# Kernel tuning notes

Hardware: AMD Instinct MI355X
Metric: run time of the kernel (lower is better)

## Reference

```python
import jax, jax.numpy as jnp
import numpy as np

GRID = (15, 15)
HW = GRID[0] * GRID[1]
IMAGE_SIZE = 240
TEMP = 0.07
EPS = 1e-12


def make_masks(h, w, k):
    grid = np.arange(h * w).reshape(h, w)
    # matches torch unfold: kernel offsets row-major, spatial positions row-major
    idx = np.stack([grid[i:i + h - k + 1, j:j + w - k + 1] for i in range(k) for j in range(k)])
    return jnp.asarray(idx.reshape(k * k, -1), dtype=jnp.int32)  # [k*k, n_masks]


def _l2n(x):
    return x / jnp.maximum(jnp.linalg.norm(x, axis=-1, keepdims=True), EPS)


def cosine_sim(a, b):
    # a: [..., N, D], b: [M, D] -> [..., N, M]
    return jnp.einsum('...nd,md->...nm', _l2n(a), _l2n(b))


def harmonic_aggregation(window_scores, masks):
    # window_scores: [B, n_masks]; masks: [k2, n_masks] flat patch indices
    n_masks = masks.shape[1]
    # membership matrix M[p, w] = 1 if patch p is covered by window w
    M = jnp.zeros((HW, n_masks), dtype=window_scores.dtype)
    M = M.at[masks, jnp.arange(n_masks)[None, :]].set(1.0)
    counts = M.sum(axis=1)                                  # [HW]
    sums = (1.0 / window_scores) @ M.T                      # [B, HW]
    scores = counts[None, :] / sums
    scores = jnp.nan_to_num(scores, nan=0.0, posinf=0.0)
    return scores.reshape(-1, GRID[0], GRID[1])


def visual_association_score(embeds, ref_embeds):
    # embeds: [B, N, D]; ref_embeds: [K, N, D]
    flat = ref_embeds.reshape(-1, embeds.shape[-1])          # [K*N, D]
    scores = cosine_sim(embeds, flat)                        # [B, N, K*N]
    return (1.0 - scores).min(axis=-1) / 2.0                 # [B, N]


def setup_inputs() -> dict:
    key = jax.random.key(0)
    ks = jax.random.split(key, 8)
    B, D, K = 256, 640, 4
    return {
        'image_embeds': jax.random.normal(ks[0], (B, D), jnp.float32),
        'window_embeds_s2': jax.random.normal(ks[1], (B, 196, D), jnp.float32),
        'window_embeds_s3': jax.random.normal(ks[2], (B, 169, D), jnp.float32),
        'patch_embeds': jax.random.normal(ks[3], (B, 225, D), jnp.float32),
        'text_embeds': jax.random.normal(ks[4], (2, D), jnp.float32),
        'ref_patch_embeds': jax.random.normal(ks[5], (K, 225, D), jnp.float32),
        'ref_window_s2': jax.random.normal(ks[6], (K, 196, D), jnp.float32),
        'ref_window_s3': jax.random.normal(ks[7], (K, 169, D), jnp.float32),
        'masks_s2': make_masks(GRID[0], GRID[1], 2),
        'masks_s3': make_masks(GRID[0], GRID[1], 3),
    }


def reference(image_embeds, window_embeds_s2, window_embeds_s3, patch_embeds,
              text_embeds, ref_patch_embeds, ref_window_s2, ref_window_s3,
              masks_s2, masks_s3):
    B = image_embeds.shape[0]
    # image-level zero-shot anomaly score
    img_probs = jax.nn.softmax(cosine_sim(image_embeds, text_embeds) / TEMP, axis=-1)
    image_scores = img_probs[..., 1]                         # [B]

    # zero-shot multi-scale (harmonic mean of image score + window scores)
    zs = [jnp.broadcast_to(image_scores[:, None, None], (B, GRID[0], GRID[1]))]
    for we, m in ((window_embeds_s2, masks_s2), (window_embeds_s3, masks_s3)):
        s = jax.nn.softmax(cosine_sim(we, text_embeds) / TEMP, axis=-1)[..., 1]  # [B, n_masks]
        zs.append(harmonic_aggregation(s, m))
    zero_shot = len(zs) / (1.0 / jnp.stack(zs)).sum(axis=0)   # [B, H, W]

    # few-shot scores
    fs = [visual_association_score(patch_embeds, ref_patch_embeds).reshape(B, GRID[0], GRID[1])]
    for we, re, m in ((window_embeds_s2, ref_window_s2, masks_s2),
                      (window_embeds_s3, ref_window_s3, masks_s3)):
        fs.append(harmonic_aggregation(visual_association_score(we, re), m))
    few_shot = jnp.stack(fs).mean(axis=0)                     # [B, H, W]

    multi_scale = (zero_shot + few_shot) / 2.0
    image_scores = (image_scores + few_shot.max(axis=(-2, -1))) / 2.0
    pixel_scores = jax.image.resize(multi_scale, (B, IMAGE_SIZE, IMAGE_SIZE), method='bilinear')
    return image_scores, pixel_scores
```

## Files before the change

### kernel.cpp

```cpp
#include <hip/hip_runtime.h>
#include <cmath>

#define D 640
#define TEMP_INV (1.0f / 0.07f)

typedef __attribute__((ext_vector_type(8))) short bf16x8;
typedef __attribute__((ext_vector_type(4))) float f32x4;

__device__ __forceinline__ short f2bf(float f) {
    unsigned int u = __float_as_uint(f);
    unsigned int r = (u + 0x7fffu + ((u >> 16) & 1u)) >> 16;
    return (short)r;
}

__device__ __forceinline__ void gload_lds16(const void* g, void* l) {
    __builtin_amdgcn_global_load_lds(
        (const __attribute__((address_space(1))) unsigned int*)g,
        (__attribute__((address_space(3))) unsigned int*)l, 16, 0, 0);
}

__global__ void textnorm_k(const float* __restrict__ T, float* __restrict__ tn) {
    int w = threadIdx.x >> 6, lane = threadIdx.x & 63;
    const float* row = T + w * D;
    float v[10]; float ss = 0.f;
#pragma unroll
    for (int i = 0; i < 10; i++) { v[i] = row[lane + 64 * i]; ss += v[i] * v[i]; }
#pragma unroll
    for (int m = 1; m < 64; m <<= 1) ss += __shfl_xor(ss, m, 64);
    float rn = 1.f / fmaxf(sqrtf(ss), 1e-12f);
#pragma unroll
    for (int i = 0; i < 10; i++) tn[w * D + lane + 64 * i] = v[i] * rn;
}

__global__ __launch_bounds__(256) void normstore_k(
    const float* __restrict__ X, int nsrc, int npad, const float* __restrict__ tn,
    float* __restrict__ score_out, short* __restrict__ bf16_out) {
    int wid = blockIdx.x * 4 + (threadIdx.x >> 6);
    int lane = threadIdx.x & 63;
    if (wid >= npad) return;
    const float2* row = (const float2*)(X + (size_t)(wid < nsrc ? wid : 0) * D);
    const float2* t0 = (const float2*)tn;
    const float2* t1 = (const float2*)(tn + D);
    float2 v[5]; float ss = 0.f, d0 = 0.f, d1 = 0.f;
#pragma unroll
    for (int i = 0; i < 5; i++) {
        float2 a = row[lane + 64 * i];
        v[i] = a;
        ss += a.x * a.x + a.y * a.y;
        if (tn) {
            float2 b0 = t0[lane + 64 * i], b1 = t1[lane + 64 * i];
            d0 += a.x * b0.x + a.y * b0.y;
            d1 += a.x * b1.x + a.y * b1.y;
        }
    }
#pragma unroll
    for (int m = 1; m < 64; m <<= 1) {
        ss += __shfl_xor(ss, m, 64);
        if (tn) { d0 += __shfl_xor(d0, m, 64); d1 += __shfl_xor(d1, m, 64); }
    }
    float rn = 1.f / fmaxf(sqrtf(ss), 1e-12f);
    if (score_out && lane == 0)
        score_out[wid] = 1.f / (1.f + expf(-((d1 - d0) * rn) * TEMP_INV));
    if (bf16_out) {
        ushort2* o = (ushort2*)bf16_out;
#pragma unroll
        for (int i = 0; i < 5; i++) {
            ushort2 p;
            p.x = (unsigned short)f2bf(v[i].x * rn);
            p.y = (unsigned short)f2bf(v[i].y * rn);
            o[(size_t)wid * 320 + lane + 64 * i] = p;
        }
    }
}

__global__ __launch_bounds__(512, 4) void gemm_max_k(
    const short* __restrict__ A, const short* __restrict__ B,
    int nch, int U, float* __restrict__ partial) {
    __shared__ short Al[128 * 64];
    __shared__ short Bl[256 * 64];
    const int t = threadIdx.x;
    const int g = blockIdx.x & 7, ii = blockIdx.x >> 3;
    const int ulo = (int)(((long long)g * U) >> 3);
    const int uhi = (int)(((long long)(g + 1) * U) >> 3);
    const int S = uhi - ulo;
    if (ii >= S) return;
    const int cnt = (S - ii + 63) >> 6;
    const int nchq = nch * 4;

    const int srow = t >> 3;
    const int scol = (t & 7) * 16;
    const int gsw = (scol ^ ((srow & 7) << 4)) >> 1;

    const int lane = t & 63, wave = t >> 6;
    const int l15 = lane & 15, lhi = lane >> 4;
    const int wr = wave >> 2, wc = wave & 3;
    const int xk = (l15 & 7) << 4;

    char* Ab = (char*)Al;
    char* Bb = (char*)Bl;
    char* Ad = Ab + srow * 128 + scol;
    char* Bd = Bb + srow * 128 + scol;

    for (int j = 0; j < cnt; j++) {
        const int u = ulo + ii + (j << 6);
        const int rc = u / nch, nc = u - rc * nch;
        const short* Ag = A + ((size_t)rc * 128 + srow) * D + gsw;
        const short* Bg = B + ((size_t)nc * 256 + srow) * D + gsw;

        f32x4 acc[4][4];
#pragma unroll
        for (int m = 0; m < 4; m++)
#pragma unroll
            for (int n = 0; n < 4; n++) acc[m][n] = (f32x4){0.f, 0.f, 0.f, 0.f};

        for (int ks = 0; ks < 10; ks++) {
            const int k0 = ks * 64;
            __syncthreads();
#pragma unroll
            for (int i = 0; i < 2; i++)
                gload_lds16(Ag + k0 + (size_t)(i * 64) * D, Ad + i * 8192);
#pragma unroll
            for (int i = 0; i < 4; i++)
                gload_lds16(Bg + k0 + (size_t)(i * 64) * D, Bd + i * 8192);
            __syncthreads();
#pragma unroll
            for (int sub = 0; sub < 2; sub++) {
                const int kbs = (sub * 64 + lhi * 16) ^ xk;
                bf16x8 a[4], b[4];
#pragma unroll
                for (int m = 0; m < 4; m++)
                    a[m] = *(const bf16x8*)(Ab + (wr * 64 + m * 16 + l15) * 128 + kbs);
#pragma unroll
                for (int n = 0; n < 4; n++)
                    b[n] = *(const bf16x8*)(Bb + (wc * 64 + n * 16 + l15) * 128 + kbs);
#pragma unroll
                for (int m = 0; m < 4; m++)
#pragma unroll
                    for (int n = 0; n < 4; n++)
                        acc[m][n] = __builtin_amdgcn_mfma_f32_16x16x32_bf16(a[m], b[n], acc[m][n], 0, 0, 0);
            }
        }

#pragma unroll
        for (int m = 0; m < 4; m++)
#pragma unroll
            for (int r = 0; r < 4; r++) {
                float v = fmaxf(fmaxf(acc[m][0][r], acc[m][1][r]),
                                fmaxf(acc[m][2][r], acc[m][3][r]));
#pragma unroll
                for (int msk = 1; msk < 16; msk <<= 1)
                    v = fmaxf(v, __shfl_xor(v, msk, 64));
                if (l15 == 0) {
                    int row = rc * 128 + wr * 64 + m * 16 + lhi * 4 + r;
                    partial[(size_t)row * nchq + nc * 4 + wc] = v;
                }
            }
    }
}

__global__ __launch_bounds__(256) void reducemax_k(
    const float* __restrict__ partial, int nchq, int nrows, float* __restrict__ vas) {
    int r = blockIdx.x * 256 + threadIdx.x;
    if (r >= nrows) return;
    float m = -1e30f;
    for (int i = 0; i < nchq; i++) m = fmaxf(m, partial[(size_t)r * nchq + i]);
    vas[r] = (1.0f - m) * 0.5f;
}

__global__ __launch_bounds__(256) void rowstats_k(
    const float* __restrict__ X, int nrows, const float* __restrict__ tn,
    float* __restrict__ rnorm_out, float* __restrict__ score_out) {
    int wid = blockIdx.x * 4 + (threadIdx.x >> 6);
    int lane = threadIdx.x & 63;
    if (wid >= nrows) return;
    const float* row = X + (size_t)wid * D;
    float ss = 0.f, d0 = 0.f, d1 = 0.f;
#pragma unroll
    for (int i = 0; i < 10; i++) {
        float v = row[lane + 64 * i];
        ss += v * v;
        if (tn) { d0 += v * tn[lane + 64 * i]; d1 += v * tn[D + lane + 64 * i]; }
    }
#pragma unroll
    for (int m = 1; m < 64; m <<= 1) {
        ss += __shfl_xor(ss, m, 64);
        if (tn) { d0 += __shfl_xor(d0, m, 64); d1 += __shfl_xor(d1, m, 64); }
    }
    if (lane == 0) {
        float rn = 1.f / fmaxf(sqrtf(ss), 1e-12f);
        if (rnorm_out) rnorm_out[wid] = rn;
        if (score_out) score_out[wid] = 1.f / (1.f + expf(-((d1 - d0) * rn) * TEMP_INV));
    }
}

__global__ __launch_bounds__(256) void refnorm_k(
    const float* __restrict__ R, int M, int Mp, short* __restrict__ out) {
    int wid = blockIdx.x * 4 + (threadIdx.x >> 6);
    int lane = threadIdx.x & 63;
    if (wid >= Mp) return;
    const float* row = R + (size_t)(wid < M ? wid : 0) * D;
    float v[10]; float ss = 0.f;
#pragma unroll
    for (int i = 0; i < 10; i++) { v[i] = row[lane + 64 * i]; ss += v[i] * v[i]; }
#pragma unroll
    for (int m = 1; m < 64; m <<= 1) ss += __shfl_xor(ss, m, 64);
    float rn = 1.f / fmaxf(sqrtf(ss), 1e-12f);
#pragma unroll
    for (int i = 0; i < 10; i++) out[(size_t)wid * D + lane + 64 * i] = f2bf(v[i] * rn);
}

#define SA 648
#define SB 72
__global__ __launch_bounds__(256) void maxcos_k(
    const float* __restrict__ X, const float* __restrict__ rnorm,
    const short* __restrict__ refs, int Mp, float* __restrict__ vas_out) {
    __shared__ short Alds[64 * SA];
    __shared__ short Blds[64 * SB];
    const int t = threadIdx.x;
    const size_t rowBase = (size_t)blockIdx.x * 64;
#pragma unroll
    for (int i = 0; i < 20; i++) {
        int c = i * 256 + t;
        int row = c / 80, col = (c % 80) * 8;
        const float* p = X + (rowBase + row) * D + col;
        float rn = rnorm[rowBase + row];
        float4 v0 = *(const float4*)p;
        float4 v1 = *(const float4*)(p + 4);
        bf16x8 s;
        s[0] = f2bf(v0.x * rn); s[1] = f2bf(v0.y * rn);
        s[2] = f2bf(v0.z * rn); s[3] = f2bf(v0.w * rn);
        s[4] = f2bf(v1.x * rn); s[5] = f2bf(v1.y * rn);
        s[6] = f2bf(v1.z * rn); s[7] = f2bf(v1.w * rn);
        *(bf16x8*)&Alds[row * SA + col] = s;
    }
    __syncthreads();
    const int lane = t & 63, wave = t >> 6;
    const int l15 = lane & 15, lhi = lane >> 4;
    const int wr0 = wave * 16;
    float rowmax[4] = {-1e30f, -1e30f, -1e30f, -1e30f};
    for (int m0 = 0; m0 < Mp; m0 += 64) {
        f32x4 zero = {0.f, 0.f, 0.f, 0.f};
        f32x4 acc[4] = {zero, zero, zero, zero};
        for (int ks = 0; ks < 10; ks++) {
            __syncthreads();
#pragma unroll
            for (int c2 = 0; c2 < 2; c2++) {
                int c = c2 * 256 + t;
                int n = c >> 3, kk = (c & 7) * 8;
                const short* g = refs + (size_t)(m0 + n) * D + ks * 64 + kk;
                *(bf16x8*)&Blds[n * SB + kk] = *(const bf16x8*)g;
            }
            __syncthreads();
#pragma unroll
            for (int sub = 0; sub < 2; sub++) {
                bf16x8 a = *(const bf16x8*)&Alds[(wr0 + l15) * SA + ks * 64 + sub * 32 + lhi * 8];
#pragma unroll
                for (int s = 0; s < 4; s++) {
                    bf16x8 b = *(const bf16x8*)&Blds[(s * 16 + l15) * SB + sub * 32 + lhi * 8];
                    acc[s] = __builtin_amdgcn_mfma_f32_16x16x32_bf16(a, b, acc[s], 0, 0, 0);
                }
            }
        }
#pragma unroll
        for (int r = 0; r < 4; r++) {
            float mv = fmaxf(fmaxf(acc[0][r], acc[1][r]), fmaxf(acc[2][r], acc[3][r]));
#pragma unroll
            for (int msk = 1; msk < 16; msk <<= 1) mv = fmaxf(mv, __shfl_xor(mv, msk, 64));
            rowmax[r] = fmaxf(rowmax[r], mv);
        }
    }
    if (l15 == 0) {
#pragma unroll
        for (int r = 0; r < 4; r++) {
            size_t row = rowBase + wr0 + lhi * 4 + r;
            vas_out[row] = (1.0f - rowmax[r]) * 0.5f;
        }
    }
}

__global__ __launch_bounds__(256) void fuse_k(
    const float* __restrict__ imgsc, const float* __restrict__ zs2,
    const float* __restrict__ zs3, const float* __restrict__ vasP,
    const float* __restrict__ vas2, const float* __restrict__ vas3,
    float* __restrict__ multi, float* __restrict__ img_out) {
    int b = blockIdx.x, t = threadIdx.x;
    __shared__ float red[256];
    float few = -1e30f;
    if (t < 225) {
        int i = t / 15, j = t % 15;
        float invz2 = 0.f, invf2 = 0.f; int c2 = 0;
        int ilo = max(0, i - 1), ihi = min(i, 13), jlo = max(0, j - 1), jhi = min(j, 13);
        for (int i0 = ilo; i0 <= ihi; i0++)
            for (int j0 = jlo; j0 <= jhi; j0++) {
                int w = b * 196 + i0 * 14 + j0;
                invz2 += 1.f / zs2[w]; invf2 += 1.f / vas2[w]; c2++;
            }
        float zh2 = (float)c2 / invz2, fh2 = (float)c2 / invf2;
        float invz3 = 0.f, invf3 = 0.f; int c3 = 0;
        ilo = max(0, i - 2); ihi = min(i, 12); jlo = max(0, j - 2); jhi = min(j, 12);
        for (int i0 = ilo; i0 <= ihi; i0++)
            for (int j0 = jlo; j0 <= jhi; j0++) {
                int w = b * 169 + i0 * 13 + j0;
                invz3 += 1.f / zs3[w]; invf3 += 1.f / vas3[w]; c3++;
            }
        float zh3 = (float)c3 / invz3, fh3 = (float)c3 / invf3;
        float is = imgsc[b];
        float zero_shot = 3.f / (1.f / is + 1.f / zh2 + 1.f / zh3);
        float fs0 = vasP[b * 225 + t];
        few = (fs0 + fh2 + fh3) * (1.f / 3.f);
        multi[b * 225 + t] = (zero_shot + few) * 0.5f;
    }
    red[t] = few;
    __syncthreads();
    for (int s = 128; s > 0; s >>= 1) {
        if (t < s) red[t] = fmaxf(red[t], red[t + s]);
        __syncthreads();
    }
    if (t == 0) img_out[b] = (imgsc[b] + red[0]) * 0.5f;
}

__global__ __launch_bounds__(256) void resize_k(
    const float* __restrict__ multi, float* __restrict__ out) {
    int idx = blockIdx.x * 256 + threadIdx.x;
    int x = idx % 240;
    int rest = idx / 240;
    int y = rest % 240;
    int b = rest / 240;
    float sx = (x + 0.5f) * 0.0625f - 0.5f;
    float sy = (y + 0.5f) * 0.0625f - 0.5f;
    sx = fminf(fmaxf(sx, 0.f), 14.f);
    sy = fminf(fmaxf(sy, 0.f), 14.f);
    int x0 = min((int)sx, 13), y0 = min((int)sy, 13);
    float fx = sx - x0, fy = sy - y0;
    const float* m = multi + b * 225;
    float v00 = m[y0 * 15 + x0],      v01 = m[y0 * 15 + x0 + 1];
    float v10 = m[y0 * 15 + 15 + x0], v11 = m[y0 * 15 + 15 + x0 + 1];
    out[idx] = (1.f - fy) * ((1.f - fx) * v00 + fx * v01)
             + fy * ((1.f - fx) * v10 + fx * v11);
}

extern "C" void kernel_launch(void* const* d_in, const int* in_sizes, int n_in,
                              void* d_out, int out_size, void* d_ws, size_t ws_size,
                              hipStream_t stream) {
    const float* image = (const float*)d_in[0];
    const float* w2    = (const float*)d_in[1];
    const float* w3    = (const float*)d_in[2];
    const float* patch = (const float*)d_in[3];
    const float* text  = (const float*)d_in[4];
    const float* refP  = (const float*)d_in[5];
    const float* ref2  = (const float*)d_in[6];
    const float* ref3  = (const float*)d_in[7];
    float* out_img = (float*)d_out;
    float* out_pix = out_img + 256;

    char* wsb = (char*)d_ws;
    size_t off = 0;
    auto alloc = [&](size_t bytes) -> void* {
        void* p = wsb + off;
        off += (bytes + 255) & ~(size_t)255;
        return p;
    };

    const size_t NEW_NEED = 72300000;
    if (ws_size >= NEW_NEED) {
        float* tn    = (float*)alloc(2 * 640 * 4);
        float* imgsc = (float*)alloc(256 * 4);
        float* zs2   = (float*)alloc(50176 * 4);
        float* zs3   = (float*)alloc(43264 * 4);
        short* nrefP = (short*)alloc(1024 * 640 * 2);
        short* nref2 = (short*)alloc(1024 * 640 * 2);
        short* nref3 = (short*)alloc(768 * 640 * 2);
        short* Abuf  = (short*)alloc((size_t)50176 * 640 * 2);
        float* partial = (float*)alloc((size_t)50176 * 16 * 4);
        float* vasP  = (float*)alloc(57600 * 4);
        float* vas2  = (float*)alloc(50176 * 4);
        float* vas3  = (float*)alloc(43264 * 4);
        float* multi = (float*)alloc(57600 * 4);

        textnorm_k<<<1, 128, 0, stream>>>(text, tn);
        normstore_k<<<64, 256, 0, stream>>>(image, 256, 256, tn, imgsc, nullptr);
        normstore_k<<<256, 256, 0, stream>>>(refP, 900, 1024, nullptr, nullptr, nrefP);
        normstore_k<<<256, 256, 0, stream>>>(ref2, 784, 1024, nullptr, nullptr, nref2);
        normstore_k<<<192, 256, 0, stream>>>(ref3, 676, 768, nullptr, nullptr, nref3);

        for (int h = 0; h < 2; h++) {
            const float* src = patch + (size_t)h * 28800 * D;
            normstore_k<<<7200, 256, 0, stream>>>(src, 28800, 28800, nullptr, nullptr, Abuf);
            gemm_max_k<<<512, 512, 0, stream>>>(Abuf, nrefP, 4, 900, partial);
            reducemax_k<<<113, 256, 0, stream>>>(partial, 16, 28800, vasP + h * 28800);
        }
        normstore_k<<<12544, 256, 0, stream>>>(w2, 50176, 50176, tn, zs2, Abuf);
        gemm_max_k<<<512, 512, 0, stream>>>(Abuf, nref2, 4, 1568, partial);
        reducemax_k<<<196, 256, 0, stream>>>(partial, 16, 50176, vas2);
        normstore_k<<<10816, 256, 0, stream>>>(w3, 43264, 43264, tn, zs3, Abuf);
        gemm_max_k<<<512, 512, 0, stream>>>(Abuf, nref3, 3, 1014, partial);
        reducemax_k<<<169, 256, 0, stream>>>(partial, 12, 43264, vas3);

        fuse_k<<<256, 256, 0, stream>>>(imgsc, zs2, zs3, vasP, vas2, vas3, multi, out_img);
        resize_k<<<57600, 256, 0, stream>>>(multi, out_pix);
    } else {
        float* tn    = (float*)alloc(2 * 640 * 4);
        float* imgsc = (float*)alloc(256 * 4);
        float* rn2   = (float*)alloc(50176 * 4);
        float* rn3   = (float*)alloc(43264 * 4);
        float* rnp   = (float*)alloc(57600 * 4);
        float* zs2   = (float*)alloc(50176 * 4);
        float* zs3   = (float*)alloc(43264 * 4);
        short* nrefP = (short*)alloc(960 * 640 * 2);
        short* nref2 = (short*)alloc(832 * 640 * 2);
        short* nref3 = (short*)alloc(704 * 640 * 2);
        float* vasP  = (float*)alloc(57600 * 4);
        float* vas2  = (float*)alloc(50176 * 4);
        float* vas3  = (float*)alloc(43264 * 4);
        float* multi = (float*)alloc(57600 * 4);

        textnorm_k<<<1, 128, 0, stream>>>(text, tn);
        rowstats_k<<<64, 256, 0, stream>>>(image, 256, tn, nullptr, imgsc);
        rowstats_k<<<12544, 256, 0, stream>>>(w2, 50176, tn, rn2, zs2);
        rowstats_k<<<10816, 256, 0, stream>>>(w3, 43264, tn, rn3, zs3);
        rowstats_k<<<14400, 256, 0, stream>>>(patch, 57600, nullptr, rnp, nullptr);
        refnorm_k<<<240, 256, 0, stream>>>(refP, 900, 960, nrefP);
        refnorm_k<<<208, 256, 0, stream>>>(ref2, 784, 832, nref2);
        refnorm_k<<<176, 256, 0, stream>>>(ref3, 676, 704, nref3);
        maxcos_k<<<900, 256, 0, stream>>>(patch, rnp, nrefP, 960, vasP);
        maxcos_k<<<784, 256, 0, stream>>>(w2, rn2, nref2, 832, vas2);
        maxcos_k<<<676, 256, 0, stream>>>(w3, rn3, nref3, 704, vas3);
        fuse_k<<<256, 256, 0, stream>>>(imgsc, zs2, zs3, vasP, vas2, vas3, multi, out_img);
        resize_k<<<57600, 256, 0, stream>>>(multi, out_pix);
    }
}
```

Baseline: 392.1 us.

## Triple-buffer LDS tiles in gemm_max_k with a flattened persistent pipeline

The GEMM-max kernel moves from a single LDS buffer with two barriers per k-step to a three-stage ring. Global-to-LDS loads run two tiles ahead, and a vmcnt wait plus one barrier guards each step. The output-tile and k loops are flattened into one stream so prefetch carries across tile boundaries. The grid is halved to 256 blocks, each handling twice the work, and launch bounds drop occupancy to 2 because LDS use is now about 144KB per block. The aim is to hide load latency behind MFMA work, at the cost of fewer resident blocks and a possible tail imbalance.

Result: slower. 494.5 us (+26.1%).

```diff
diff --git a/kernel.cpp b/kernel.cpp
--- a/kernel.cpp
+++ b/kernel.cpp
@@ -73,18 +73,19 @@
     }
 }
 
-__global__ __launch_bounds__(512, 4) void gemm_max_k(
+__global__ __launch_bounds__(512, 2) void gemm_max_k(
     const short* __restrict__ A, const short* __restrict__ B,
     int nch, int U, float* __restrict__ partial) {
-    __shared__ short Al[128 * 64];
-    __shared__ short Bl[256 * 64];
+    __shared__ short Al[3][128 * 64];
+    __shared__ short Bl[3][256 * 64];
     const int t = threadIdx.x;
     const int g = blockIdx.x & 7, ii = blockIdx.x >> 3;
     const int ulo = (int)(((long long)g * U) >> 3);
     const int uhi = (int)(((long long)(g + 1) * U) >> 3);
-    const int S = uhi - ulo;
-    if (ii >= S) return;
-    const int cnt = (S - ii + 63) >> 6;
+    int cnt = uhi - ulo - ii;
+    cnt = (cnt > 0) ? (cnt + 31) >> 5 : 0;
+    const int T = cnt * 10;
+    if (T <= 0) return;
     const int nchq = nch * 4;
 
     const int srow = t >> 3;
@@ -96,65 +97,84 @@
     const int wr = wave >> 2, wc = wave & 3;
     const int xk = (l15 & 7) << 4;
 
-    char* Ab = (char*)Al;
-    char* Bb = (char*)Bl;
-    char* Ad = Ab + srow * 128 + scol;
-    char* Bd = Bb + srow * 128 + scol;
-
-    for (int j = 0; j < cnt; j++) {
-        const int u = ulo + ii + (j << 6);
-        const int rc = u / nch, nc = u - rc * nch;
-        const short* Ag = A + ((size_t)rc * 128 + srow) * D + gsw;
-        const short* Bg = B + ((size_t)nc * 256 + srow) * D + gsw;
-
-        f32x4 acc[4][4];
-#pragma unroll
-        for (int m = 0; m < 4; m++)
-#pragma unroll
-            for (int n = 0; n < 4; n++) acc[m][n] = (f32x4){0.f, 0.f, 0.f, 0.f};
-
-        for (int ks = 0; ks < 10; ks++) {
-            const int k0 = ks * 64;
-            __syncthreads();
-#pragma unroll
-            for (int i = 0; i < 2; i++)
-                gload_lds16(Ag + k0 + (size_t)(i * 64) * D, Ad + i * 8192);
-#pragma unroll
-            for (int i = 0; i < 4; i++)
-                gload_lds16(Bg + k0 + (size_t)(i * 64) * D, Bd + i * 8192);
-            __syncthreads();
-#pragma unroll
-            for (int sub = 0; sub < 2; sub++) {
-                const int kbs = (sub * 64 + lhi * 16) ^ xk;
-                bf16x8 a[4], b[4];
-#pragma unroll
-                for (int m = 0; m < 4; m++)
-                    a[m] = *(const bf16x8*)(Ab + (wr * 64 + m * 16 + l15) * 128 + kbs);
+    auto coords = [&](int tile, int& rc, int& nc, int& ks) {
+        int uj = tile / 10; ks = tile - uj * 10;
+        int u = ulo + ii + 32 * uj;
+        rc = u / nch; nc = u - rc * nch;
+    };
+
+    auto stage = [&](int buf, int tile) {
+        int rc, nc, ks; coords(tile, rc, nc, ks);
+        const short* Ag = A + ((size_t)rc * 128 + srow) * D + ks * 64 + gsw;
+        const short* Bg = B + ((size_t)nc * 256 + srow) * D + ks * 64 + gsw;
+        char* Ad = (char*)&Al[buf][0] + srow * 128 + scol;
+        char* Bd = (char*)&Bl[buf][0] + srow * 128 + scol;
+#pragma unroll
+        for (int i = 0; i < 2; i++)
+            gload_lds16(Ag + (size_t)(i * 64) * D, Ad + i * 8192);
+#pragma unroll
+        for (int i = 0; i < 4; i++)
+            gload_lds16(Bg + (size_t)(i * 64) * D, Bd + i * 8192);
+    };
+
+    f32x4 acc[4][4];
+#pragma unroll
+    for (int m = 0; m < 4; m++)
+#pragma unroll
+        for (int n = 0; n < 4; n++) acc[m][n] = (f32x4){0.f, 0.f, 0.f, 0.f};
+
+    stage(0, 0);
+    stage(1, 1);
+
+    for (int tt = 0; tt < T; tt++) {
+        const int cur = tt % 3;
+        asm volatile("s_waitcnt vmcnt(6)" ::: "memory");
+        __builtin_amdgcn_s_barrier();
+        asm volatile("" ::: "memory");
+
+        int nxt = tt + 2; if (nxt > T - 1) nxt = T - 1;
+        stage((tt + 2) % 3, nxt);
+
+        const char* Ab = (const char*)&Al[cur][0];
+        const char* Bb = (const char*)&Bl[cur][0];
+#pragma unroll
+        for (int sub = 0; sub < 2; sub++) {
+            const int kbs = (sub * 64 + lhi * 16) ^ xk;
+            bf16x8 a[4], b[4];
+#pragma unroll
+            for (int m = 0; m < 4; m++)
+                a[m] = *(const bf16x8*)(Ab + (wr * 64 + m * 16 + l15) * 128 + kbs);
+#pragma unroll
+            for (int n = 0; n < 4; n++)
+                b[n] = *(const bf16x8*)(Bb + (wc * 64 + n * 16 + l15) * 128 + kbs);
+#pragma unroll
+            for (int m = 0; m < 4; m++)
 #pragma unroll
                 for (int n = 0; n < 4; n++)
-                    b[n] = *(const bf16x8*)(Bb + (wc * 64 + n * 16 + l15) * 128 + kbs);
-#pragma unroll
-                for (int m = 0; m < 4; m++)
-#pragma unroll
-                    for (int n = 0; n < 4; n++)
-                        acc[m][n] = __builtin_amdgcn_mfma_f32_16x16x32_bf16(a[m], b[n], acc[m][n], 0, 0, 0);
-            }
-        }
-
-#pragma unroll
-        for (int m = 0; m < 4; m++)
-#pragma unroll
-            for (int r = 0; r < 4; r++) {
-                float v = fmaxf(fmaxf(acc[m][0][r], acc[m][1][r]),
-                                fmaxf(acc[m][2][r], acc[m][3][r]));
-#pragma unroll
-                for (int msk = 1; msk < 16; msk <<= 1)
-                    v = fmaxf(v, __shfl_xor(v, msk, 64));
-                if (l15 == 0) {
-                    int row = rc * 128 + wr * 64 + m * 16 + lhi * 4 + r;
-                    partial[(size_t)row * nchq + nc * 4 + wc] = v;
+                    acc[m][n] = __builtin_amdgcn_mfma_f32_16x16x32_bf16(a[m], b[n], acc[m][n], 0, 0, 0);
+        }
+
+        if (tt % 10 == 9) {
+            int rc, nc, k9; coords(tt, rc, nc, k9);
+#pragma unroll
+            for (int m = 0; m < 4; m++)
+#pragma unroll
+                for (int r = 0; r < 4; r++) {
+                    float v = fmaxf(fmaxf(acc[m][0][r], acc[m][1][r]),
+                                    fmaxf(acc[m][2][r], acc[m][3][r]));
+#pragma unroll
+                    for (int msk = 1; msk < 16; msk <<= 1)
+                        v = fmaxf(v, __shfl_xor(v, msk, 64));
+                    if (l15 == 0) {
+                        int row = rc * 128 + wr * 64 + m * 16 + lhi * 4 + r;
+                        partial[(size_t)row * nchq + nc * 4 + wc] = v;
+                    }
                 }
-            }
+#pragma unroll
+            for (int m = 0; m < 4; m++)
+#pragma unroll
+                for (int n = 0; n < 4; n++) acc[m][n] = (f32x4){0.f, 0.f, 0.f, 0.f};
+        }
     }
 }
 
@@ -386,14 +406,14 @@
         for (int h = 0; h < 2; h++) {
             const float* src = patch + (size_t)h * 28800 * D;
             normstore_k<<<7200, 256, 0, stream>>>(src, 28800, 28800, nullptr, nullptr, Abuf);
-            gemm_max_k<<<512, 512, 0, stream>>>(Abuf, nrefP, 4, 900, partial);
+            gemm_max_k<<<256, 512, 0, stream>>>(Abuf, nrefP, 4, 900, partial);
             reducemax_k<<<113, 256, 0, stream>>>(partial, 16, 28800, vasP + h * 28800);
         }
         normstore_k<<<12544, 256, 0, stream>>>(w2, 50176, 50176, tn, zs2, Abuf);
-        gemm_max_k<<<512, 512, 0, stream>>>(Abuf, nref2, 4, 1568, partial);
+        gemm_max_k<<<256, 512, 0, stream>>>(Abuf, nref2, 4, 1568, partial);
         reducemax_k<<<196, 256, 0, stream>>>(partial, 16, 50176, vas2);
         normstore_k<<<10816, 256, 0, stream>>>(w3, 43264, 43264, tn, zs3, Abuf);
-        gemm_max_k<<<512, 512, 0, stream>>>(Abuf, nref3, 3, 1014, partial);
+        gemm_max_k<<<256, 512, 0, stream>>>(Abuf, nref3, 3, 1014, partial);
         reducemax_k<<<169, 256, 0, stream>>>(partial, 12, 43264, vas3);
 
         fuse_k<<<256, 256, 0, stream>>>(imgsc, zs2, zs3, vasP, vas2, vas3, multi, out_img);
```

## Triple-buffer GEMM LDS loads with one tile per block

Applied to the files above, without the earlier changes.

Rewrites the bf16 MFMA GEMM-max kernel to use a 3-stage LDS ring with 32-wide K slices. Global-to-LDS loads for step k+2 are issued while step k computes, synchronised with a manual vmcnt wait and a single barrier per step. The persistent loop over tiles is replaced by a grid of one block per output tile, so launch sizes grow to cover all tiles. This aims to hide memory latency behind MFMA work, at the cost of more blocks, a new swizzle, and hand-tuned waitcnt logic that could be fragile.

After: 422.5 us. 1.08x slower.

```diff
diff --git a/kernel.cpp b/kernel.cpp
--- a/kernel.cpp
+++ b/kernel.cpp
@@ -76,86 +76,82 @@
 __global__ __launch_bounds__(512, 4) void gemm_max_k(
     const short* __restrict__ A, const short* __restrict__ B,
     int nch, int U, float* __restrict__ partial) {
-    __shared__ short Al[128 * 64];
-    __shared__ short Bl[256 * 64];
+    __shared__ short Al[3][128 * 32];
+    __shared__ short Bl[3][256 * 32];
     const int t = threadIdx.x;
     const int g = blockIdx.x & 7, ii = blockIdx.x >> 3;
     const int ulo = (int)(((long long)g * U) >> 3);
     const int uhi = (int)(((long long)(g + 1) * U) >> 3);
-    const int S = uhi - ulo;
-    if (ii >= S) return;
-    const int cnt = (S - ii + 63) >> 6;
+    const int u = ulo + ii;
+    if (u >= uhi) return;
+    const int rc = u / nch, nc = u - rc * nch;
     const int nchq = nch * 4;
 
-    const int srow = t >> 3;
-    const int scol = (t & 7) * 16;
-    const int gsw = (scol ^ ((srow & 7) << 4)) >> 1;
+    const int srow = t >> 2;
+    const int scol = (t & 3) * 16;
+    const int gsw = (scol ^ (((t >> 3) & 3) << 4)) >> 1;
 
     const int lane = t & 63, wave = t >> 6;
     const int l15 = lane & 15, lhi = lane >> 4;
     const int wr = wave >> 2, wc = wave & 3;
-    const int xk = (l15 & 7) << 4;
-
-    char* Ab = (char*)Al;
-    char* Bb = (char*)Bl;
-    char* Ad = Ab + srow * 128 + scol;
-    char* Bd = Bb + srow * 128 + scol;
-
-    for (int j = 0; j < cnt; j++) {
-        const int u = ulo + ii + (j << 6);
-        const int rc = u / nch, nc = u - rc * nch;
-        const short* Ag = A + ((size_t)rc * 128 + srow) * D + gsw;
-        const short* Bg = B + ((size_t)nc * 256 + srow) * D + gsw;
-
-        f32x4 acc[4][4];
+    const int kb = (lhi * 16) ^ (((l15 >> 1) & 3) << 4);
+
+    const short* Ag = A + ((size_t)rc * 128 + srow) * D + gsw;
+    const short* Bg = B + ((size_t)nc * 256 + srow) * D + gsw;
+
+    auto stage = [&](int buf, int ks) {
+        gload_lds16(Ag + ks * 32, (char*)&Al[buf][0] + t * 16);
+        gload_lds16(Bg + ks * 32, (char*)&Bl[buf][0] + t * 16);
+        gload_lds16(Bg + (size_t)128 * D + ks * 32, (char*)&Bl[buf][0] + 8192 + t * 16);
+    };
+
+    f32x4 acc[4][4];
+#pragma unroll
+    for (int m = 0; m < 4; m++)
+#pragma unroll
+        for (int n = 0; n < 4; n++) acc[m][n] = (f32x4){0.f, 0.f, 0.f, 0.f};
+
+    stage(0, 0);
+    stage(1, 1);
+
+    for (int ks = 0; ks < 20; ks++) {
+        asm volatile("s_waitcnt vmcnt(3)" ::: "memory");
+        __builtin_amdgcn_s_barrier();
+        asm volatile("" ::: "memory");
+
+        int nxt = ks + 2; if (nxt > 19) nxt = 19;
+        stage((ks + 2) % 3, nxt);
+
+        const char* Ab = (const char*)&Al[ks % 3][0];
+        const char* Bb = (const char*)&Bl[ks % 3][0];
+        bf16x8 a[4], b[4];
 #pragma unroll
         for (int m = 0; m < 4; m++)
-#pragma unroll
-            for (int n = 0; n < 4; n++) acc[m][n] = (f32x4){0.f, 0.f, 0.f, 0.f};
-
-        for (int ks = 0; ks < 10; ks++) {
-            const int k0 = ks * 64;
-            __syncthreads();
-#pragma unroll
-            for (int i = 0; i < 2; i++)
-                gload_lds16(Ag + k0 + (size_t)(i * 64) * D, Ad + i * 8192);
-#pragma unroll
-            for (int i = 0; i < 4; i++)
-                gload_lds16(Bg + k0 + (size_t)(i * 64) * D, Bd + i * 8192);
-            __syncthreads();
-#pragma unroll
-            for (int sub = 0; sub < 2; sub++) {
-                const int kbs = (sub * 64 + lhi * 16) ^ xk;
-                bf16x8 a[4], b[4];
-#pragma unroll
-                for (int m = 0; m < 4; m++)
-                    a[m] = *(const bf16x8*)(Ab + (wr * 64 + m * 16 + l15) * 128 + kbs);
-#pragma unroll
-                for (int n = 0; n < 4; n++)
-                    b[n] = *(const bf16x8*)(Bb + (wc * 64 + n * 16 + l15) * 128 + kbs);
-#pragma unroll
-                for (int m = 0; m < 4; m++)
-#pragma unroll
-                    for (int n = 0; n < 4; n++)
-                        acc[m][n] = __builtin_amdgcn_mfma_f32_16x16x32_bf16(a[m], b[n], acc[m][n], 0, 0, 0);
+            a[m] = *(const bf16x8*)(Ab + (wr * 64 + m * 16 + l15) * 64 + kb);
+#pragma unroll
+        for (int n = 0; n < 4; n++)
+            b[n] = *(const bf16x8*)(Bb + (wc * 64 + n * 16 + l15) * 64 + kb);
+#pragma unroll
+        for (int m = 0; m < 4; m++)
+#pragma unroll
+            for (int n = 0; n < 4; n++)
+                acc[m][n] = __builtin_amdgcn_mfma_f32_16x16x32_bf16(a[m], b[n], acc[m][n], 0, 0, 0);
+    }
+
+#pragma unroll
+    for (int m = 0; m < 4; m++)
+#pragma unroll
+        for (int r = 0; r < 4; r++) {
+            float v = fmaxf(fmaxf(acc[m][0][r], acc[m][1][r]),
+                            fmaxf(acc[m][2][r], acc[m][3][r]));
+#pragma unroll
+            for (int msk = 1; msk < 16; msk <<= 1)
+                v = fmaxf(v, __shfl_xor(v, msk, 64));
+            if (l15 == 0) {
+                int row = rc * 128 + wr * 64 + m * 16 + lhi * 4 + r;
+                partial[(size_t)row * nchq + nc * 4 + wc] = v;
             }
         }
-
-#pragma unroll
-        for (int m = 0; m < 4; m++)
-#pragma unroll
-            for (int r = 0; r < 4; r++) {
-                float v = fmaxf(fmaxf(acc[m][0][r], acc[m][1][r]),
-                                fmaxf(acc[m][2][r], acc[m][3][r]));
-#pragma unroll
-                for (int msk = 1; msk < 16; msk <<= 1)
-                    v = fmaxf(v, __shfl_xor(v, msk, 64));
-                if (l15 == 0) {
-                    int row = rc * 128 + wr * 64 + m * 16 + lhi * 4 + r;
-                    partial[(size_t)row * nchq + nc * 4 + wc] = v;
-                }
-            }
-    }
 }
 
 __global__ __launch_bounds__(256) void reducemax_k(
@@ -386,14 +382,14 @@
         for (int h = 0; h < 2; h++) {
             const float* src = patch + (size_t)h * 28800 * D;
             normstore_k<<<7200, 256, 0, stream>>>(src, 28800, 28800, nullptr, nullptr, Abuf);
-            gemm_max_k<<<512, 512, 0, stream>>>(Abuf, nrefP, 4, 900, partial);
+            gemm_max_k<<<904, 512, 0, stream>>>(Abuf, nrefP, 4, 900, partial);
             reducemax_k<<<113, 256, 0, stream>>>(partial, 16, 28800, vasP + h * 28800);
         }
         normstore_k<<<12544, 256, 0, stream>>>(w2, 50176, 50176, tn, zs2, Abuf);
-        gemm_max_k<<<512, 512, 0, stream>>>(Abuf, nref2, 4, 1568, partial);
+        gemm_max_k<<<1568, 512, 0, stream>>>(Abuf, nref2, 4, 1568, partial);
         reducemax_k<<<196, 256, 0, stream>>>(partial, 16, 50176, vas2);
         normstore_k<<<10816, 256, 0, stream>>>(w3, 43264, 43264, tn, zs3, Abuf);
-        gemm_max_k<<<512, 512, 0, stream>>>(Abuf, nref3, 3, 1014, partial);
+        gemm_max_k<<<1016, 512, 0, stream>>>(Abuf, nref3, 3, 1014, partial);
         reducemax_k<<<169, 256, 0, stream>>>(partial, 12, 43264, vas3);
 
         fuse_k<<<256, 256, 0, stream>>>(imgsc, zs2, zs3, vasP, vas2, vas3, multi, out_img);
```
